# Kernel optimization log

Hardware: AMD Instinct MI355X
Metric: run time of the kernel (lower is better)

## Reference

```python
import jax, jax.numpy as jnp
import numpy as np
import math

D_MODEL = 256
PRED_LEN = 256
K = 32
LOW_FREQ = 1


def setup_inputs() -> dict:
    key = jax.random.key(0)
    x = jax.random.normal(key, (8, 1024, D_MODEL), dtype=jnp.float32)
    return {"x": x}


def reference(x):
    """x: (b, t, d) -> reconstructed/extrapolated series (b, t+pred_len, d)."""
    b, t, d = x.shape
    k_ = K  # K < t//2, so the explicit-k branch of the torch module is taken

    x_freq = jnp.fft.rfft(x, axis=1)  # (b, t//2+1, d) complex
    if t % 2 == 0:
        x_freq_high = x_freq[:, LOW_FREQ:-1]  # drop DC..low_freq-1 and Nyquist
    else:
        x_freq_high = x_freq[:, LOW_FREQ:]

    # top-k magnitudes over the frequency axis, independently per (b, d)
    mag = jnp.abs(x_freq_high)                                   # (b, F, d)
    _, idx = jax.lax.top_k(jnp.transpose(mag, (0, 2, 1)), k_)    # (b, d, k)
    idx = jnp.transpose(idx, (0, 2, 1)) + LOW_FREQ               # (b, k, d) into x_freq

    x_freq_topk = jnp.take_along_axis(x_freq, idx, axis=1)       # (b, k, d) complex
    freqs = jnp.fft.rfftfreq(t).astype(x.dtype)                  # (t//2+1,)
    f_topk = freqs[idx]                                          # (b, k, d)

    # append conjugate / negative-frequency pair for a real reconstruction
    x_ext = jnp.concatenate([x_freq_topk, jnp.conj(x_freq_topk)], axis=1)  # (b, 2k, d)
    f_ext = jnp.concatenate([f_topk, -f_topk], axis=1)                     # (b, 2k, d)

    t_val = jnp.arange(t + PRED_LEN, dtype=x.dtype)              # (T,)
    amp = (jnp.abs(x_ext) / t)[:, :, None, :]                    # (b, 2k, 1, d)
    phase = jnp.angle(x_ext)[:, :, None, :]                      # (b, 2k, 1, d)
    arg = (2.0 * math.pi) * f_ext[:, :, None, :] * t_val[None, None, :, None] + phase
    x_time = amp * jnp.cos(arg)                                  # (b, 2k, T, d)
    return jnp.sum(x_time, axis=1)                               # (b, T, d)
```

## Files before the change

### kernel.cpp

```cpp
#include <hip/hip_runtime.h>
#include <math.h>

#define T_LEN 1024
#define PRED_LEN 256
#define OUT_T (T_LEN + PRED_LEN)
#define DM 256
#define KSEL 32
#define RTAU 1e-4f

#define PAD16(i) ((i) + ((i) >> 4))
#define C1024F 0.006135923151542565f

__device__ __constant__ float W16RF[16] = {
    1.0f,  0.92387953f,  0.70710678f,  0.38268343f, 0.0f, -0.38268343f, -0.70710678f, -0.92387953f,
   -1.0f, -0.92387953f, -0.70710678f, -0.38268343f, 0.0f,  0.38268343f,  0.70710678f,  0.92387953f };
__device__ __constant__ float W16IF[16] = {
    0.0f, -0.38268343f, -0.70710678f, -0.92387953f, -1.0f, -0.92387953f, -0.70710678f, -0.38268343f,
    0.0f,  0.38268343f,  0.70710678f,  0.92387953f,  1.0f,  0.92387953f,  0.70710678f,  0.38268343f };

#define C1_ 0.92387953251128675613
#define C2_ 0.70710678118654752440
#define C3_ 0.38268343236508977173
__device__ __constant__ double W16R_[16] = {
    1.0,  C1_,  C2_,  C3_, 0.0, -C3_, -C2_, -C1_,
   -1.0, -C1_, -C2_, -C3_, 0.0,  C3_,  C2_,  C1_ };
__device__ __constant__ double W16I_[16] = {
    0.0, -C3_, -C2_, -C1_, -1.0, -C1_, -C2_, -C3_,
    0.0,  C3_,  C2_,  C1_,  1.0,  C1_,  C2_,  C3_ };

template<bool PADDED>
__device__ __forceinline__ void fft1024(const float2* __restrict__ xin,
                                        const float2* __restrict__ twF,
                                        int lane, int w, float* ar, float* ai) {
    float Fr[4][4], Fi[4][4];
#pragma unroll
    for (int n1a = 0; n1a < 4; ++n1a) {
        int i0 = lane + 64 * (n1a + 0);
        int i1 = lane + 64 * (n1a + 4);
        int i2 = lane + 64 * (n1a + 8);
        int i3 = lane + 64 * (n1a + 12);
        float2 a  = xin[PADDED ? PAD16(i0) : i0];
        float2 bb = xin[PADDED ? PAD16(i1) : i1];
        float2 cV = xin[PADDED ? PAD16(i2) : i2];
        float2 d  = xin[PADDED ? PAD16(i3) : i3];
        float t0r = a.x + cV.x, t0i = a.y + cV.y;
        float t1r = a.x - cV.x, t1i = a.y - cV.y;
        float t2r = bb.x + d.x, t2i = bb.y + d.y;
        float t3r = bb.x - d.x, t3i = bb.y - d.y;
        Fr[n1a][0] = t0r + t2r;  Fi[n1a][0] = t0i + t2i;
        Fr[n1a][2] = t0r - t2r;  Fi[n1a][2] = t0i - t2i;
        Fr[n1a][1] = t1r + t3i;  Fi[n1a][1] = t1i - t3r;
        Fr[n1a][3] = t1r - t3i;  Fi[n1a][3] = t1i + t3r;
    }
#pragma unroll
    for (int q = 0; q < 4; ++q) {
        const int k1 = (w << 2) | q;
        float cr = Fr[0][q], ci = Fi[0][q];
#pragma unroll
        for (int n1a = 1; n1a < 4; ++n1a) {
            int e = (n1a * k1) & 15;
            float wr = W16RF[e], wi = W16IF[e];
            cr += Fr[n1a][q] * wr - Fi[n1a][q] * wi;
            ci += Fr[n1a][q] * wi + Fi[n1a][q] * wr;
        }
        float2 tw = twF[PAD16((lane * k1) & 1023)];
        ar[q] = cr * tw.x - ci * tw.y;
        ai[q] = cr * tw.y + ci * tw.x;
    }
#pragma unroll
    for (int s = 0; s < 6; ++s) {
        const int half = 32 >> s;
        const int e = (lane & (half - 1)) << s;
        float2 tw = twF[PAD16(e << 4)];
        const bool up = (lane & half) != 0;
#pragma unroll
        for (int q = 0; q < 4; ++q) {
            float orr = __shfl_xor(ar[q], half);
            float oii = __shfl_xor(ai[q], half);
            float sr = ar[q] + orr, si = ai[q] + oii;
            float dr = orr - ar[q], di = oii - ai[q];
            ar[q] = up ? (dr * tw.x - di * tw.y) : sr;
            ai[q] = up ? (dr * tw.y + di * tw.x) : si;
        }
    }
}

__global__ void __launch_bounds__(256, 4)
fl_fused_kernel(const float* __restrict__ x, float* __restrict__ out) {
    __shared__ float2 twF[PAD16(1023) + 1];
    __shared__ float2 spP[PAD16(1023) + 1];
    __shared__ char smemU[8192];
    __shared__ int hist[512];
    __shared__ unsigned selw[32];
    float2* xsh  = (float2*)smemU;
    float2* xunp = (float2*)smemU;

    const int tid  = threadIdx.x;
    const int lane = tid & 63;
    const int w    = tid >> 6;

    const int bid = blockIdx.x;
    const int sp  = ((bid & 7) << 7) | (bid >> 3);
    const int b   = sp >> 7;
    const int d0  = (sp & 127) << 1;

    for (int j = 0; j < 4; ++j) {
        int e = tid + (j << 8);
        float sn, cs;
        __sincosf((float)e * C1024F, &sn, &cs);
        twF[PAD16(e)] = float2{ cs, -sn };
        xsh[e] = *reinterpret_cast<const float2*>(&x[(((size_t)(b << 10) + e) << 8) + d0]);
    }
    if (tid < 32) selw[tid] = 0u;
    __syncthreads();

    float ar[4], ai[4];
    fft1024<false>(xsh, twF, lane, w, ar, ai);

    const int krev = (int)(__brev((unsigned)lane) >> 26);
#pragma unroll
    for (int q = 0; q < 4; ++q) {
        int k = ((w << 2) | q) + (krev << 4);
        spP[PAD16(k)] = float2{ ar[q], ai[q] };
    }
    __syncthreads();

    if (tid < 128) {
        const int c = tid >> 6;
        int* histc = hist + (c << 8);

        float v[8]; int hiw[8];
#pragma unroll
        for (int q = 0; q < 8; ++q) {
            int m = (q << 6) | lane;
            int n = (1024 - m) & 1023;
            float2 Pk = spP[PAD16(m)];
            float2 Pn = spP[PAD16(n)];
            float rr, ii;
            if (c == 0) { rr = 0.5f * (Pk.x + Pn.x); ii = 0.5f * (Pk.y - Pn.y); }
            else        { rr = 0.5f * (Pk.y + Pn.y); ii = 0.5f * (Pn.x - Pk.x); }
            v[q] = rr * rr + ii * ii;
        }
        if (lane == 0) v[0] = -1.0f;
#pragma unroll
        for (int q = 0; q < 8; ++q) hiw[q] = __float_as_int(v[q]);

        int mx = hiw[0];
#pragma unroll
        for (int q = 1; q < 8; ++q) mx = max(mx, hiw[q]);
#pragma unroll
        for (int off = 1; off < 64; off <<= 1) mx = max(mx, __shfl_xor(mx, off));

        const int base = (mx >> 20) - 250;
        int idx[8];
#pragma unroll
        for (int q = 0; q < 8; ++q) {
            int t = (hiw[q] >> 20) - base;
            idx[q] = t < 0 ? 0 : t;
        }

        *reinterpret_cast<int4*>(&histc[lane << 2]) = int4{0, 0, 0, 0};
#pragma unroll
        for (int q = 0; q < 8; ++q) atomicAdd(&histc[idx[q]], 1);

        int4 cc = *reinterpret_cast<int4*>(&histc[lane << 2]);
        int s_local = cc.x + cc.y + cc.z + cc.w;

        int s = s_local;
#pragma unroll
        for (int off = 1; off < 64; off <<= 1) {
            int t = __shfl_down(s, off);
            if (lane + off < 64) s += t;
        }
        const int S_gt = s - s_local;
        const int A3 = S_gt;
        const int A2 = A3 + cc.w;
        const int A1 = A2 + cc.z;
        const int A0 = A1 + cc.y;

        int foundB = -1, foundR = 0;
        if (A0 < KSEL && A0 + cc.x >= KSEL) { foundB = (lane << 2) | 0; foundR = KSEL - A0; }
        if (A1 < KSEL && A1 + cc.y >= KSEL) { foundB = (lane << 2) | 1; foundR = KSEL - A1; }
        if (A2 < KSEL && A2 + cc.z >= KSEL) { foundB = (lane << 2) | 2; foundR = KSEL - A2; }
        if (A3 < KSEL && A3 + cc.w >= KSEL) { foundB = (lane << 2) | 3; foundR = KSEL - A3; }

        unsigned long long fm = __ballot(foundB >= 0);
        const int srcB = (int)(__ffsll((unsigned long long)fm) - 1);
        const int B = __shfl(foundB, srcB);
        const int r = __shfl(foundR, srcB);

        unsigned selmask = 0, candmask = 0;
#pragma unroll
        for (int q = 0; q < 8; ++q) {
            if (idx[q] > B) selmask |= (1u << q);
            else if (idx[q] == B) candmask |= (1u << q);
        }

        for (int it = 0; it < r; ++it) {
            float bv = -2.0f; int bq = -1;
#pragma unroll
            for (int q = 0; q < 8; ++q) {
                bool cand = ((candmask >> q) & 1u) != 0;
                if (cand && v[q] > bv) { bv = v[q]; bq = q; }
            }
            int bi = (bq < 0) ? 0x7FFFFFFF : ((bq << 6) | lane);
#pragma unroll
            for (int off = 1; off < 64; off <<= 1) {
                float ov = __shfl_xor(bv, off);
                int   oi = __shfl_xor(bi, off);
                if (ov > bv || (ov == bv && oi < bi)) { bv = ov; bi = oi; }
            }
            if (bi != 0x7FFFFFFF && lane == (bi & 63)) {
                unsigned bit = 1u << (bi >> 6);
                selmask  |= bit;
                candmask &= ~bit;
            }
        }

        {
            float vminS = 3.0e38f, vmaxU = -3.0e38f;
#pragma unroll
            for (int q = 0; q < 8; ++q) {
                if ((selmask >> q) & 1u) vminS = fminf(vminS, v[q]);
                else                     vmaxU = fmaxf(vmaxU, v[q]);
            }
#pragma unroll
            for (int off = 1; off < 64; off <<= 1) {
                vminS = fminf(vminS, __shfl_xor(vminS, off));
                vmaxU = fmaxf(vmaxU, __shfl_xor(vmaxU, off));
            }
            const float tau = RTAU * vminS;
            if (vminS - vmaxU < tau) {
                const float lo = vmaxU - tau, hi = vminS + tau;
                unsigned candq = 0; int nAbove = 0;
#pragma unroll
                for (int q = 0; q < 8; ++q) {
                    bool inw = (v[q] >= lo) && (v[q] <= hi);
                    if (inw) candq |= (1u << q);
                    if (((selmask >> q) & 1u) && v[q] > hi) ++nAbove;
                }
#pragma unroll
                for (int off = 1; off < 64; off <<= 1) nAbove += __shfl_xor(nAbove, off);
                const int kneed = KSEL - nAbove;
                selmask &= ~candq;

                const float* xcol = x + ((size_t)(b << 10) << 8) + d0 + c;
                double sV = -1.0; int sSrc = 0; int cnum = 0;
                for (int q = 0; q < 8; ++q) {
                    unsigned long long bal = __ballot((candq >> q) & 1u);
                    while (bal) {
                        int srcl = (int)(__ffsll(bal) - 1);
                        bal &= bal - 1;
                        int m = (q << 6) | srcl;
                        double th0 = (double)((m * lane) & 1023)
                                   * (-6.283185307179586476925286766559 / 1024.0);
                        double wr, wi;
                        { double s0, c0; sincos(th0, &s0, &c0); wr = c0; wi = s0; }
                        const double stR = W16R_[m & 15], stI = W16I_[m & 15];
                        double sr = 0.0, si = 0.0;
#pragma unroll
                        for (int u = 0; u < 16; ++u) {
                            int n = lane + (u << 6);
                            double xvd = (double)xcol[(size_t)n << 8];
                            sr = fma(xvd, wr, sr);
                            si = fma(xvd, wi, si);
                            double nwr = wr * stR - wi * stI;
                            double nwi = wr * stI + wi * stR;
                            wr = nwr; wi = nwi;
                        }
#pragma unroll
                        for (int off = 1; off < 64; off <<= 1) {
                            sr += __shfl_xor(sr, off);
                            si += __shfl_xor(si, off);
                        }
                        if (lane == cnum) { sV = sr * sr + si * si; sSrc = (q << 6) | srcl; }
                        ++cnum;
                        if (cnum >= 64) break;
                    }
                    if (cnum >= 64) break;
                }
                for (int it = 0; it < kneed; ++it) {
                    double bv = sV; int bl = lane;
#pragma unroll
                    for (int off = 1; off < 64; off <<= 1) {
                        double ov = __shfl_xor(bv, off);
                        int    ol = __shfl_xor(bl, off);
                        if (ov > bv || (ov == bv && ol < bl)) { bv = ov; bl = ol; }
                    }
                    int wsrc = __shfl(sSrc, bl);
                    if (lane == (wsrc & 63)) selmask |= 1u << (wsrc >> 6);
                    if (lane == bl) sV = -2.0;
                }
            }
        }

#pragma unroll
        for (int q = 0; q < 8; ++q) {
            if ((selmask >> q) & 1u) {
                int m = (q << 6) | lane;
                atomicOr(&selw[(c << 4) | (m >> 5)], 1u << (m & 31));
            }
        }
    } else {
        const int t2 = tid - 128;
#pragma unroll
        for (int j = 0; j < 4; ++j) {
            int k = t2 + (j << 7);
            int n = (1024 - k) & 1023;
            float2 Pk = spP[PAD16(k)];
            float2 Pn = spP[PAD16(n)];
            xunp[k]       = float2{ 0.5f * (Pk.x + Pn.x), 0.5f * (Pk.y - Pn.y) };
            xunp[512 + k] = float2{ 0.5f * (Pk.y + Pn.y), 0.5f * (Pn.x - Pk.x) };
        }
    }
    __syncthreads();

#pragma unroll
    for (int jj = 0; jj < 4; ++jj) {
        int k = tid + (jj << 8);
        float2 z{ 0.0f, 0.0f };
        if (k != 0 && k != 512) {
            int fold = (k < 512) ? k : (1024 - k);
            float sgn = (k < 512) ? 1.0f : -1.0f;
            float2 X0 = xunp[fold];
            float2 X1 = xunp[512 + fold];
            X0.y *= sgn; X1.y *= sgn;
            bool s0 = (selw[fold >> 5]        >> (fold & 31)) & 1u;
            bool s1 = (selw[16 + (fold >> 5)] >> (fold & 31)) & 1u;
            float Zr = (s0 ? X0.x : 0.0f) - (s1 ? X1.y : 0.0f);
            float Zi = (s0 ? X0.y : 0.0f) + (s1 ? X1.x : 0.0f);
            z = float2{ Zr, -Zi };
        }
        spP[PAD16(k)] = z;
    }
    __syncthreads();

    fft1024<true>(spP, twF, lane, w, ar, ai);

    {
        const float S = 1.0f / 1024.0f;
        float2* o2 = reinterpret_cast<float2*>(out + (size_t)b * OUT_T * DM + d0);
#pragma unroll
        for (int q = 0; q < 4; ++q) {
            int t = ((w << 2) | q) + (krev << 4);
            float2 o{ ar[q] * S, -ai[q] * S };
            o2[(size_t)t * 128] = o;
            if (t < PRED_LEN) o2[(size_t)(t + T_LEN) * 128] = o;
        }
    }
}

extern "C" void kernel_launch(void* const* d_in, const int* in_sizes, int n_in,
                              void* d_out, int out_size, void* d_ws, size_t ws_size,
                              hipStream_t stream) {
    const float* x = (const float*)d_in[0];
    float* out = (float*)d_out;
    hipLaunchKernelGGL(fl_fused_kernel, dim3(1024), dim3(256), 0, stream, x, out);
}
```

Measured before the change: 36.27 us.

## Fuse spectrum masking into inverse FFT loads and add second radix pass for ties

Result: faster. 35.36 us (-2.5%).

```diff
diff --git a/kernel.cpp b/kernel.cpp
--- a/kernel.cpp
+++ b/kernel.cpp
@@ -28,21 +28,85 @@
     0.0, -C3_, -C2_, -C1_, -1.0, -C1_, -C2_, -C3_,
     0.0,  C3_,  C2_,  C1_,  1.0,  C1_,  C2_,  C3_ };
 
-template<bool PADDED>
+__device__ __forceinline__ float2 zval(const float2* __restrict__ xunp,
+                                       const unsigned* __restrict__ selw, int k) {
+    if (k == 0 || k == 512) return float2{ 0.f, 0.f };
+    const int  fold = (k < 512) ? k : (1024 - k);
+    const float sgn = (k < 512) ? 1.0f : -1.0f;
+    float2 X0 = xunp[fold];
+    float2 X1 = xunp[512 + fold];
+    const bool s0 = (selw[fold >> 5]        >> (fold & 31)) & 1u;
+    const bool s1 = (selw[16 + (fold >> 5)] >> (fold & 31)) & 1u;
+    float x0i = sgn * X0.y;
+    float x1i = sgn * X1.y;
+    float Zr = (s0 ? X0.x : 0.f) - (s1 ? x1i : 0.f);
+    float Zi = (s0 ? x0i : 0.f) + (s1 ? X1.x : 0.f);
+    return float2{ Zr, -Zi };
+}
+
 __device__ __forceinline__ void fft1024(const float2* __restrict__ xin,
                                         const float2* __restrict__ twF,
                                         int lane, int w, float* ar, float* ai) {
     float Fr[4][4], Fi[4][4];
 #pragma unroll
     for (int n1a = 0; n1a < 4; ++n1a) {
-        int i0 = lane + 64 * (n1a + 0);
-        int i1 = lane + 64 * (n1a + 4);
-        int i2 = lane + 64 * (n1a + 8);
-        int i3 = lane + 64 * (n1a + 12);
-        float2 a  = xin[PADDED ? PAD16(i0) : i0];
-        float2 bb = xin[PADDED ? PAD16(i1) : i1];
-        float2 cV = xin[PADDED ? PAD16(i2) : i2];
-        float2 d  = xin[PADDED ? PAD16(i3) : i3];
+        float2 a  = xin[lane + 64 * (n1a + 0)];
+        float2 bb = xin[lane + 64 * (n1a + 4)];
+        float2 cV = xin[lane + 64 * (n1a + 8)];
+        float2 d  = xin[lane + 64 * (n1a + 12)];
+        float t0r = a.x + cV.x, t0i = a.y + cV.y;
+        float t1r = a.x - cV.x, t1i = a.y - cV.y;
+        float t2r = bb.x + d.x, t2i = bb.y + d.y;
+        float t3r = bb.x - d.x, t3i = bb.y - d.y;
+        Fr[n1a][0] = t0r + t2r;  Fi[n1a][0] = t0i + t2i;
+        Fr[n1a][2] = t0r - t2r;  Fi[n1a][2] = t0i - t2i;
+        Fr[n1a][1] = t1r + t3i;  Fi[n1a][1] = t1i - t3r;
+        Fr[n1a][3] = t1r - t3i;  Fi[n1a][3] = t1i + t3r;
+    }
+#pragma unroll
+    for (int q = 0; q < 4; ++q) {
+        const int k1 = (w << 2) | q;
+        float cr = Fr[0][q], ci = Fi[0][q];
+#pragma unroll
+        for (int n1a = 1; n1a < 4; ++n1a) {
+            int e = (n1a * k1) & 15;
+            float wr = W16RF[e], wi = W16IF[e];
+            cr += Fr[n1a][q] * wr - Fi[n1a][q] * wi;
+            ci += Fr[n1a][q] * wi + Fi[n1a][q] * wr;
+        }
+        float2 tw = twF[PAD16((lane * k1) & 1023)];
+        ar[q] = cr * tw.x - ci * tw.y;
+        ai[q] = cr * tw.y + ci * tw.x;
+    }
+#pragma unroll
+    for (int s = 0; s < 6; ++s) {
+        const int half = 32 >> s;
+        const int e = (lane & (half - 1)) << s;
+        float2 tw = twF[PAD16(e << 4)];
+        const bool up = (lane & half) != 0;
+#pragma unroll
+        for (int q = 0; q < 4; ++q) {
+            float orr = __shfl_xor(ar[q], half);
+            float oii = __shfl_xor(ai[q], half);
+            float sr = ar[q] + orr, si = ai[q] + oii;
+            float dr = orr - ar[q], di = oii - ai[q];
+            ar[q] = up ? (dr * tw.x - di * tw.y) : sr;
+            ai[q] = up ? (dr * tw.y + di * tw.x) : si;
+        }
+    }
+}
+
+__device__ __forceinline__ void fft1024_z(const float2* __restrict__ xunp,
+                                          const unsigned* __restrict__ selw,
+                                          const float2* __restrict__ twF,
+                                          int lane, int w, float* ar, float* ai) {
+    float Fr[4][4], Fi[4][4];
+#pragma unroll
+    for (int n1a = 0; n1a < 4; ++n1a) {
+        float2 a  = zval(xunp, selw, lane + 64 * (n1a + 0));
+        float2 bb = zval(xunp, selw, lane + 64 * (n1a + 4));
+        float2 cV = zval(xunp, selw, lane + 64 * (n1a + 8));
+        float2 d  = zval(xunp, selw, lane + 64 * (n1a + 12));
         float t0r = a.x + cV.x, t0i = a.y + cV.y;
         float t1r = a.x - cV.x, t1i = a.y - cV.y;
         float t2r = bb.x + d.x, t2i = bb.y + d.y;
@@ -115,7 +179,7 @@
     __syncthreads();
 
     float ar[4], ai[4];
-    fft1024<false>(xsh, twF, lane, w, ar, ai);
+    fft1024(xsh, twF, lane, w, ar, ai);
 
     const int krev = (int)(__brev((unsigned)lane) >> 26);
 #pragma unroll
@@ -186,14 +250,55 @@
 
         unsigned long long fm = __ballot(foundB >= 0);
         const int srcB = (int)(__ffsll((unsigned long long)fm) - 1);
-        const int B = __shfl(foundB, srcB);
-        const int r = __shfl(foundR, srcB);
+        int B = __shfl(foundB, srcB);
+        int r = __shfl(foundR, srcB);
 
         unsigned selmask = 0, candmask = 0;
 #pragma unroll
         for (int q = 0; q < 8; ++q) {
             if (idx[q] > B) selmask |= (1u << q);
             else if (idx[q] == B) candmask |= (1u << q);
+        }
+
+        if (r > 0 && B > 0) {
+            *reinterpret_cast<int4*>(&histc[lane << 2]) = int4{0, 0, 0, 0};
+            int idx2[8];
+#pragma unroll
+            for (int q = 0; q < 8; ++q) {
+                idx2[q] = (hiw[q] >> 12) & 255;
+                if ((candmask >> q) & 1u) atomicAdd(&histc[idx2[q]], 1);
+            }
+            int4 c2 = *reinterpret_cast<int4*>(&histc[lane << 2]);
+            int s2l = c2.x + c2.y + c2.z + c2.w;
+            int ss = s2l;
+#pragma unroll
+            for (int off = 1; off < 64; off <<= 1) {
+                int t = __shfl_down(ss, off);
+                if (lane + off < 64) ss += t;
+            }
+            const int G3 = ss - s2l;
+            const int G2 = G3 + c2.w;
+            const int G1 = G2 + c2.z;
+            const int G0 = G1 + c2.y;
+            int fB2 = -1, fR2 = 0;
+            if (G0 < r && G0 + c2.x >= r) { fB2 = (lane << 2) | 0; fR2 = r - G0; }
+            if (G1 < r && G1 + c2.y >= r) { fB2 = (lane << 2) | 1; fR2 = r - G1; }
+            if (G2 < r && G2 + c2.z >= r) { fB2 = (lane << 2) | 2; fR2 = r - G2; }
+            if (G3 < r && G3 + c2.w >= r) { fB2 = (lane << 2) | 3; fR2 = r - G3; }
+            unsigned long long fm2 = __ballot(fB2 >= 0);
+            const int src2 = (int)(__ffsll((unsigned long long)fm2) - 1);
+            const int Bb = __shfl(fB2, src2);
+            const int rr = __shfl(fR2, src2);
+            unsigned newcand = 0;
+#pragma unroll
+            for (int q = 0; q < 8; ++q) {
+                if ((candmask >> q) & 1u) {
+                    if (idx2[q] > Bb) selmask |= (1u << q);
+                    else if (idx2[q] == Bb) newcand |= (1u << q);
+                }
+            }
+            candmask = newcand;
+            r = rr;
         }
 
         for (int it = 0; it < r; ++it) {
@@ -315,27 +420,7 @@
     }
     __syncthreads();
 
-#pragma unroll
-    for (int jj = 0; jj < 4; ++jj) {
-        int k = tid + (jj << 8);
-        float2 z{ 0.0f, 0.0f };
-        if (k != 0 && k != 512) {
-            int fold = (k < 512) ? k : (1024 - k);
-            float sgn = (k < 512) ? 1.0f : -1.0f;
-            float2 X0 = xunp[fold];
-            float2 X1 = xunp[512 + fold];
-            X0.y *= sgn; X1.y *= sgn;
-            bool s0 = (selw[fold >> 5]        >> (fold & 31)) & 1u;
-            bool s1 = (selw[16 + (fold >> 5)] >> (fold & 31)) & 1u;
-            float Zr = (s0 ? X0.x : 0.0f) - (s1 ? X1.y : 0.0f);
-            float Zi = (s0 ? X0.y : 0.0f) + (s1 ? X1.x : 0.0f);
-            z = float2{ Zr, -Zi };
-        }
-        spP[PAD16(k)] = z;
-    }
-    __syncthreads();
-
-    fft1024<true>(spP, twF, lane, w, ar, ai);
+    fft1024_z(xunp, selw, twF, lane, w, ar, ai);
 
     {
         const float S = 1.0f / 1024.0f;
```
